# Kernel optimization log

Hardware: AMD Instinct MI355X
Metric: run time of the kernel (lower is better)

## Reference

```python
import jax, jax.numpy as jnp
import numpy as np

N = 50000   # nodes
E = 800000  # edges (avg degree 16)
D = 64      # input_nf = output_nf = hidden_nf


def lrelu(x):
    # nn.LeakyReLU(0.2)
    return jnp.where(x >= 0, x, 0.2 * x)


def setup_inputs() -> dict:
    key = jax.random.key(0)
    ks = jax.random.split(key, 12)
    def lin(k, fan_in, fan_out):
        s = 1.0 / np.sqrt(fan_in)
        return jax.random.uniform(k, (fan_in, fan_out), jnp.float32, -s, s)
    inp = {
        "h": jax.random.normal(ks[0], (N, D), jnp.float32),
        "coord": jax.random.normal(ks[1], (N, 3), jnp.float32),
        "edge_index": jax.random.randint(ks[2], (2, E), 0, N, jnp.int32),
        # edge_mlp: Linear(2D+1, D) -> lrelu -> Linear(D, D) -> lrelu
        "w1e": lin(ks[3], 2 * D + 1, D), "b1e": jnp.zeros((D,), jnp.float32),
        "w2e": lin(ks[4], D, D),         "b2e": jnp.zeros((D,), jnp.float32),
        # node_mlp: Linear(2D, D) -> lrelu -> Linear(D, D)
        "w1n": lin(ks[5], 2 * D, D),     "b1n": jnp.zeros((D,), jnp.float32),
        "w2n": lin(ks[6], D, D),         "b2n": jnp.zeros((D,), jnp.float32),
    }
    return inp


def reference(h, coord, edge_index, w1e, b1e, w2e, b2e, w1n, b1n, w2n, b2n):
    row, col = edge_index[0], edge_index[1]
    # coord2radial
    coord_diff = coord[row] - coord[col]                    # [E, 3]
    radial = jnp.sum(coord_diff ** 2, axis=1, keepdims=True)  # [E, 1]
    # edge_model: concat(h[row], h[col], radial) -> MLP
    e_in = jnp.concatenate([h[row], h[col], radial], axis=1)  # [E, 2D+1]
    e = lrelu(e_in @ w1e + b1e)
    edge_feat = lrelu(e @ w2e + b2e)                        # [E, D]
    # node_model: unsorted_segment_sum over row, then MLP, residual
    agg = jax.ops.segment_sum(edge_feat, row, num_segments=N)  # [N, D]
    n_in = jnp.concatenate([h, agg], axis=1)                # [N, 2D]
    out = lrelu(n_in @ w1n + b1n) @ w2n + b2n               # [N, D]
    h_out = h + out                                         # residual=True
    # coords_weight == 0.0 -> coord passes through unchanged
    return (h_out, coord, edge_feat)
```

## Files before the change

### kernel.cpp

```cpp
#include <hip/hip_runtime.h>

#define NN 50000
#define NE 800000
#define D 64
#define SCAN_B 1024
#define NB ((NN + SCAN_B - 1) / SCAN_B)
#define TILES 5
#define WAVES 8
#define EPB (16 * TILES * WAVES)

typedef __attribute__((ext_vector_type(8))) short bf16x8;
typedef __attribute__((ext_vector_type(4))) float f32x4;
typedef __attribute__((ext_vector_type(4))) unsigned int u32x4;

__device__ __forceinline__ float lrelu(float x) { return x >= 0.0f ? x : 0.2f * x; }

__device__ __forceinline__ unsigned short f2bf(float f) {
    unsigned int x = __float_as_uint(f);
    unsigned int r = (x + 0x7fffu + ((x >> 16) & 1u)) >> 16;
    return (unsigned short)r;
}

__device__ __forceinline__ void wave_lds_fence() {
    asm volatile("s_waitcnt lgkmcnt(0)" ::: "memory");
    __builtin_amdgcn_sched_barrier(0);
}

__global__ __launch_bounds__(256) void prep_count(const float* __restrict__ h,
                                                  unsigned short* __restrict__ hb,
                                                  const int* __restrict__ ei,
                                                  int* __restrict__ counts,
                                                  const float* __restrict__ w1e,
                                                  const float* __restrict__ w2e,
                                                  const float* __restrict__ w1n,
                                                  const float* __restrict__ w2n,
                                                  unsigned short* __restrict__ w1t,
                                                  unsigned short* __restrict__ w2t,
                                                  unsigned short* __restrict__ w1nt,
                                                  unsigned short* __restrict__ w2nt)
{
    int i = blockIdx.x * 256 + threadIdx.x;
    float4 v = ((const float4*)h)[i];
    ushort4 o;
    o.x = f2bf(v.x); o.y = f2bf(v.y); o.z = f2bf(v.z); o.w = f2bf(v.w);
    ((ushort4*)hb)[i] = o;
    atomicAdd(&counts[ei[i]], 1);
    if (i < 8192) {
        int j = i >> 7, k = i & 127;
        w1t[i] = f2bf(w1e[k * 64 + j]);
    } else if (i < 12288) {
        int t2 = i - 8192;
        int j = t2 >> 6, k = t2 & 63;
        w2t[t2] = f2bf(w2e[k * 64 + j]);
    } else if (i < 20480) {
        int t3 = i - 12288;
        int j = t3 >> 7, k = t3 & 127;
        w1nt[t3] = f2bf(w1n[k * 64 + j]);
    } else if (i < 24576) {
        int t4 = i - 20480;
        int j = t4 >> 6, k = t4 & 63;
        w2nt[t4] = f2bf(w2n[k * 64 + j]);
    }
}

__global__ __launch_bounds__(SCAN_B) void scan_block_kernel(const int* __restrict__ counts,
                                                            int* __restrict__ offs,
                                                            int* __restrict__ bsums)
{
    int i = blockIdx.x * SCAN_B + threadIdx.x;
    int v = (i < NN) ? counts[i] : 0;
    int lane = threadIdx.x & 63;
    int wid = threadIdx.x >> 6;
    int x = v;
#pragma unroll
    for (int d = 1; d < 64; d <<= 1) {
        int y = __shfl_up(x, d);
        if (lane >= d) x += y;
    }
    __shared__ int wsum[16];
    if (lane == 63) wsum[wid] = x;
    __syncthreads();
    if (wid == 0) {
        int s = (lane < 16) ? wsum[lane] : 0;
#pragma unroll
        for (int d = 1; d < 16; d <<= 1) {
            int y = __shfl_up(s, d);
            if (lane >= d) s += y;
        }
        if (lane < 16) wsum[lane] = s;
    }
    __syncthreads();
    int woff = (wid == 0) ? 0 : wsum[wid - 1];
    int excl = woff + x - v;
    if (i < NN) offs[i] = excl;
    if (threadIdx.x == 0) bsums[blockIdx.x] = wsum[15];
}

__global__ void scan_top_kernel(int* __restrict__ bsums)
{
    if (threadIdx.x == 0 && blockIdx.x == 0) {
        int run = 0;
        for (int b = 0; b < NB; b++) { int t = bsums[b]; bsums[b] = run; run += t; }
    }
}

__global__ __launch_bounds__(SCAN_B) void add_back_kernel(int* __restrict__ offs,
                                                          const int* __restrict__ bsums,
                                                          int* __restrict__ cursor)
{
    int i = blockIdx.x * SCAN_B + threadIdx.x;
    if (i < NN) {
        int o = offs[i] + bsums[blockIdx.x];
        offs[i] = o;
        cursor[i] = o;
    }
}

__global__ __launch_bounds__(256) void scatter_kernel(const int* __restrict__ ei,
                                                      int* __restrict__ cursor,
                                                      int* __restrict__ csr,
                                                      int* __restrict__ rowpos,
                                                      int* __restrict__ colv)
{
    int e = blockIdx.x * 256 + threadIdx.x;
    if (e < NE) {
        int r = ei[e];
        int pos = atomicAdd(&cursor[r], 1);
        csr[pos] = e;
        rowpos[pos] = r;
        colv[pos] = ei[NE + e];
    }
}

__global__ __launch_bounds__(512, 2) void egnn_edge_mfma(
    const unsigned short* __restrict__ hb, const float* __restrict__ coord,
    const int* __restrict__ csr, const int* __restrict__ rowpos,
    const int* __restrict__ colv,
    const unsigned short* __restrict__ w1t, const float* __restrict__ b1e,
    const float* __restrict__ w1e,
    const unsigned short* __restrict__ w2t, const float* __restrict__ b2e,
    float* __restrict__ edge_feat, float* __restrict__ agg)
{
    __shared__ unsigned short W1[64 * 128];
    __shared__ unsigned short W2[64 * 64];
    __shared__ unsigned short Mb[WAVES][16 * 64];
    __shared__ float Ob[WAVES][16 * 64];

    const int t = threadIdx.x;
    const int orig = blockIdx.x;
    const int xcd = orig & 7, idx8 = orig >> 3;
    const int blk = (xcd < 2 ? xcd * 157 : 2 * 157 + (xcd - 2) * 156) + idx8;

    const int lane = t & 63, wv = t >> 6;
    const int lo = lane & 15, hi = lane >> 4;

    for (int c = t; c < 1024; c += 512) {
        int j = c >> 4, ci = c & 15;
        uint4 v = *(const uint4*)(w1t + j * 128 + ci * 8);
        *(uint4*)((char*)W1 + ((j * 256 + ci * 16) ^ ((j & 7) << 4))) = v;
    }
    for (int c = t; c < 512; c += 512) {
        int j = c >> 3, ci = c & 7;
        uint4 v = *(const uint4*)(w2t + j * 64 + ci * 8);
        *(uint4*)((char*)W2 + ((j * 128 + ci * 16) ^ ((j & 7) << 4))) = v;
    }
    float bj1[4], wl1[4], bj2[4];
#pragma unroll
    for (int ct = 0; ct < 4; ct++) {
        bj1[ct] = b1e[ct * 16 + lo];
        wl1[ct] = w1e[128 * 64 + ct * 16 + lo];
        bj2[ct] = b2e[ct * 16 + lo];
    }
    __syncthreads();

    char* w1b = (char*)W1;
    char* w2b = (char*)W2;
    char* mb = (char*)Mb[wv];
    char* ob = (char*)Ob[wv];

    const int pbase = blk * EPB + wv * (16 * TILES);

    int e5[TILES], row5[TILES], col5[TILES];
    float rad5[TILES];
#pragma unroll
    for (int tl = 0; tl < TILES; tl++) {
        int p = pbase + tl * 16 + lo;
        e5[tl] = csr[p];
        row5[tl] = rowpos[p];
        col5[tl] = colv[p];
    }
#pragma unroll
    for (int tl = 0; tl < TILES; tl++) {
        float dx = coord[row5[tl] * 3 + 0] - coord[col5[tl] * 3 + 0];
        float dy = coord[row5[tl] * 3 + 1] - coord[col5[tl] * 3 + 1];
        float dz = coord[row5[tl] * 3 + 2] - coord[col5[tl] * 3 + 2];
        rad5[tl] = dx * dx + dy * dy + dz * dz;
    }

    uint4 aR0, aR1, aC0, aC1, nR0, nR1, nC0, nC1;
    aR0 = *(const uint4*)(hb + (size_t)row5[0] * 64 + hi * 8);
    aR1 = *(const uint4*)(hb + (size_t)row5[0] * 64 + 32 + hi * 8);
    aC0 = *(const uint4*)(hb + (size_t)col5[0] * 64 + hi * 8);
    aC1 = *(const uint4*)(hb + (size_t)col5[0] * 64 + 32 + hi * 8);

#pragma unroll
    for (int tl = 0; tl < TILES; tl++) {
        if (tl + 1 < TILES) {
            nR0 = *(const uint4*)(hb + (size_t)row5[tl + 1] * 64 + hi * 8);
            nR1 = *(const uint4*)(hb + (size_t)row5[tl + 1] * 64 + 32 + hi * 8);
            nC0 = *(const uint4*)(hb + (size_t)col5[tl + 1] * 64 + hi * 8);
            nC1 = *(const uint4*)(hb + (size_t)col5[tl + 1] * 64 + 32 + hi * 8);
        }

        float radr[4];
#pragma unroll
        for (int r = 0; r < 4; r++) radr[r] = __shfl(rad5[tl], hi * 4 + r);
        f32x4 acc[4];
#pragma unroll
        for (int ct = 0; ct < 4; ct++)
#pragma unroll
            for (int r = 0; r < 4; r++) acc[ct][r] = fmaf(radr[r], wl1[ct], bj1[ct]);

        bf16x8 af0 = *reinterpret_cast<bf16x8*>(&aR0);
        bf16x8 af1 = *reinterpret_cast<bf16x8*>(&aR1);
        bf16x8 af2 = *reinterpret_cast<bf16x8*>(&aC0);
        bf16x8 af3 = *reinterpret_cast<bf16x8*>(&aC1);
#pragma unroll
        for (int kc = 0; kc < 4; kc++) {
            bf16x8 a = (kc == 0) ? af0 : (kc == 1) ? af1 : (kc == 2) ? af2 : af3;
#pragma unroll
            for (int ct = 0; ct < 4; ct++) {
                bf16x8 b = *(bf16x8*)(w1b + (((ct * 16 + lo) * 256 + kc * 64 + hi * 16) ^ ((lo & 7) << 4)));
                acc[ct] = __builtin_amdgcn_mfma_f32_16x16x32_bf16(a, b, acc[ct], 0, 0, 0);
            }
        }

#pragma unroll
        for (int ct = 0; ct < 4; ct++)
#pragma unroll
            for (int r = 0; r < 4; r++) {
                int row = hi * 4 + r;
                *(unsigned short*)(mb + ((row * 128 + (ct * 16 + lo) * 2) ^ ((row & 7) << 4))) =
                    f2bf(lrelu(acc[ct][r]));
            }
        wave_lds_fence();

        f32x4 acc2[4];
#pragma unroll
        for (int ct = 0; ct < 4; ct++)
#pragma unroll
            for (int r = 0; r < 4; r++) acc2[ct][r] = bj2[ct];
#pragma unroll
        for (int kc = 0; kc < 2; kc++) {
            bf16x8 a2 = *(bf16x8*)(mb + ((lo * 128 + kc * 64 + hi * 16) ^ ((lo & 7) << 4)));
#pragma unroll
            for (int ct = 0; ct < 4; ct++) {
                bf16x8 b = *(bf16x8*)(w2b + (((ct * 16 + lo) * 128 + kc * 64 + hi * 16) ^ ((lo & 7) << 4)));
                acc2[ct] = __builtin_amdgcn_mfma_f32_16x16x32_bf16(a2, b, acc2[ct], 0, 0, 0);
            }
        }

#pragma unroll
        for (int ct = 0; ct < 4; ct++)
#pragma unroll
            for (int r = 0; r < 4; r++) {
                int row = hi * 4 + r;
                *(float*)(ob + ((row * 256 + (ct * 16 + lo) * 4) ^ ((row & 7) << 4))) =
                    lrelu(acc2[ct][r]);
            }
        wave_lds_fence();

#pragma unroll
        for (int o = 0; o < 4; o++) {
            int ridx = o * 4 + hi;
            int ee = __shfl(e5[tl], ridx);
            u32x4 v = *(u32x4*)(ob + ((ridx * 256 + lo * 16) ^ ((ridx & 7) << 4)));
            __builtin_nontemporal_store(v, (u32x4*)(edge_feat + (size_t)ee * 64 + lo * 4));
        }
        {
            int cur = __shfl(row5[tl], 0);
            float s = *(float*)(ob + ((lane * 4) ^ 0));
#pragma unroll
            for (int ii = 1; ii < 16; ii++) {
                int r = __shfl(row5[tl], ii);
                float v = *(float*)(ob + ((ii * 256 + lane * 4) ^ ((ii & 7) << 4)));
                if (r != cur) {
                    atomicAdd(&agg[(size_t)cur * 64 + lane], s);
                    s = v; cur = r;
                } else {
                    s += v;
                }
            }
            atomicAdd(&agg[(size_t)cur * 64 + lane], s);
        }

        aR0 = nR0; aR1 = nR1; aC0 = nC0; aC1 = nC1;
    }
}

__global__ __launch_bounds__(256) void agg_node_mfma(
    const unsigned short* __restrict__ hb, const float* __restrict__ h,
    const float* __restrict__ coord, const float* __restrict__ agg,
    const unsigned short* __restrict__ w1nt, const float* __restrict__ b1n,
    const unsigned short* __restrict__ w2nt, const float* __restrict__ b2n,
    float* __restrict__ h_out, float* __restrict__ coord_out)
{
    __shared__ unsigned short Alds[64 * 128];
    __shared__ unsigned short Mlds[64 * 64];

    const int t = threadIdx.x, blk = blockIdx.x;
    const int lane = t & 63, wv = t >> 6;
    const int lo = lane & 15, hi = lane >> 4;
    const int nb = blk * 64;
    char* abase = (char*)Alds;
    char* mbase = (char*)Mlds;

    bf16x8 b1f[4], b2f[2];
#pragma unroll
    for (int kc = 0; kc < 4; kc++)
        b1f[kc] = *(const bf16x8*)(w1nt + (wv * 16 + lo) * 128 + kc * 32 + hi * 8);
#pragma unroll
    for (int kc = 0; kc < 2; kc++)
        b2f[kc] = *(const bf16x8*)(w2nt + (wv * 16 + lo) * 64 + kc * 32 + hi * 8);
    const float bj1 = b1n[wv * 16 + lo];
    const float bj2 = b2n[wv * 16 + lo];

    {
        int row = t >> 2, seg = t & 3;
        int n = min(nb + row, NN - 1);
        const uint4* src = (const uint4*)(hb + (size_t)n * 64 + seg * 16);
        int base = row * 256 + seg * 32;
        int swr = (row & 7) << 4;
        uint4 v0 = src[0], v1 = src[1];
        *(uint4*)(abase + (base ^ swr)) = v0;
        *(uint4*)(abase + ((base + 16) ^ swr)) = v1;
    }
    {
        int row = t >> 2, seg = t & 3;
        int n = min(nb + row, NN - 1);
        const float4* asrc = (const float4*)(agg + (size_t)n * 64 + seg * 16);
        float4 a0 = asrc[0], a1 = asrc[1], a2 = asrc[2], a3 = asrc[3];
        unsigned int u0 = f2bf(a0.x) | ((unsigned)f2bf(a0.y) << 16);
        unsigned int u1 = f2bf(a0.z) | ((unsigned)f2bf(a0.w) << 16);
        unsigned int u2 = f2bf(a1.x) | ((unsigned)f2bf(a1.y) << 16);
        unsigned int u3 = f2bf(a1.z) | ((unsigned)f2bf(a1.w) << 16);
        unsigned int u4 = f2bf(a2.x) | ((unsigned)f2bf(a2.y) << 16);
        unsigned int u5 = f2bf(a2.z) | ((unsigned)f2bf(a2.w) << 16);
        unsigned int u6 = f2bf(a3.x) | ((unsigned)f2bf(a3.y) << 16);
        unsigned int u7 = f2bf(a3.z) | ((unsigned)f2bf(a3.w) << 16);
        int base = row * 256 + 128 + seg * 32;
        int swr = (row & 7) << 4;
        *(uint4*)(abase + (base ^ swr)) = make_uint4(u0, u1, u2, u3);
        *(uint4*)(abase + ((base + 16) ^ swr)) = make_uint4(u4, u5, u6, u7);
    }
    __syncthreads();

    f32x4 acc[4];
#pragma unroll
    for (int rt = 0; rt < 4; rt++) {
#pragma unroll
        for (int r = 0; r < 4; r++) acc[rt][r] = bj1;
    }
#pragma unroll
    for (int kc = 0; kc < 4; kc++) {
#pragma unroll
        for (int rt = 0; rt < 4; rt++) {
            int row = rt * 16 + lo;
            bf16x8 a = *(bf16x8*)(abase + ((row * 256 + kc * 64 + hi * 16) ^ ((row & 7) << 4)));
            acc[rt] = __builtin_amdgcn_mfma_f32_16x16x32_bf16(a, b1f[kc], acc[rt], 0, 0, 0);
        }
    }
#pragma unroll
    for (int rt = 0; rt < 4; rt++) {
#pragma unroll
        for (int r = 0; r < 4; r++) {
            int row = rt * 16 + hi * 4 + r;
            *(unsigned short*)(mbase + ((row * 128 + (wv * 16 + lo) * 2) ^ ((row & 7) << 4))) =
                f2bf(lrelu(acc[rt][r]));
        }
    }
    __syncthreads();

    f32x4 acc2[4];
#pragma unroll
    for (int rt = 0; rt < 4; rt++) {
#pragma unroll
        for (int r = 0; r < 4; r++) acc2[rt][r] = bj2;
    }
#pragma unroll
    for (int kc = 0; kc < 2; kc++) {
#pragma unroll
        for (int rt = 0; rt < 4; rt++) {
            int row = rt * 16 + lo;
            bf16x8 a = *(bf16x8*)(mbase + ((row * 128 + kc * 64 + hi * 16) ^ ((row & 7) << 4)));
            acc2[rt] = __builtin_amdgcn_mfma_f32_16x16x32_bf16(a, b2f[kc], acc2[rt], 0, 0, 0);
        }
    }
#pragma unroll
    for (int rt = 0; rt < 4; rt++) {
#pragma unroll
        for (int r = 0; r < 4; r++) {
            int row = rt * 16 + hi * 4 + r;
            int n = nb + row;
            if (n < NN) {
                int c = wv * 16 + lo;
                float v = h[(size_t)n * 64 + c] + acc2[rt][r];
                __builtin_nontemporal_store(v, h_out + (size_t)n * 64 + c);
            }
        }
    }

    if (t < 192) {
        int idx = nb * 3 + t;
        if (idx < NN * 3) coord_out[idx] = coord[idx];
    }
}

extern "C" void kernel_launch(void* const* d_in, const int* in_sizes, int n_in,
                              void* d_out, int out_size, void* d_ws, size_t ws_size,
                              hipStream_t stream)
{
    const float* h     = (const float*)d_in[0];
    const float* coord = (const float*)d_in[1];
    const int*   ei    = (const int*)d_in[2];
    const float* w1e   = (const float*)d_in[3];
    const float* b1e   = (const float*)d_in[4];
    const float* w2e   = (const float*)d_in[5];
    const float* b2e   = (const float*)d_in[6];
    const float* w1n   = (const float*)d_in[7];
    const float* b1n   = (const float*)d_in[8];
    const float* w2n   = (const float*)d_in[9];
    const float* b2n   = (const float*)d_in[10];

    float* out       = (float*)d_out;
    float* h_out     = out;
    float* coord_out = out + (size_t)NN * D;
    float* edge_feat = coord_out + (size_t)NN * 3;

    char* ws = (char*)d_ws;
    unsigned short* hb   = (unsigned short*)ws;  ws += sizeof(unsigned short) * (size_t)NN * D;
    unsigned short* w1t  = (unsigned short*)ws;  ws += sizeof(unsigned short) * 64 * 128;
    unsigned short* w2t  = (unsigned short*)ws;  ws += sizeof(unsigned short) * 64 * 64;
    unsigned short* w1nt = (unsigned short*)ws;  ws += sizeof(unsigned short) * 64 * 128;
    unsigned short* w2nt = (unsigned short*)ws;  ws += sizeof(unsigned short) * 64 * 64;
    float* agg  = (float*)ws;                    ws += sizeof(float) * (size_t)NN * D;
    int* counts = (int*)ws;                      ws += sizeof(int) * NN;
    int* offs   = (int*)ws;                      ws += sizeof(int) * NN;
    int* cursor = (int*)ws;                      ws += sizeof(int) * NN;
    int* bsums  = (int*)ws;                      ws += sizeof(int) * 64;
    int* csr    = (int*)ws;                      ws += sizeof(int) * NE;
    int* rowpos = (int*)ws;                      ws += sizeof(int) * NE;
    int* colv   = (int*)ws;                      ws += sizeof(int) * NE;

    hipMemsetAsync(counts, 0, sizeof(int) * NN, stream);
    hipMemsetAsync(agg, 0, sizeof(float) * (size_t)NN * D, stream);

    prep_count<<<NE / 256, 256, 0, stream>>>(h, hb, ei, counts,
                                             w1e, w2e, w1n, w2n, w1t, w2t, w1nt, w2nt);

    scan_block_kernel<<<NB, SCAN_B, 0, stream>>>(counts, offs, bsums);
    scan_top_kernel<<<1, 64, 0, stream>>>(bsums);
    add_back_kernel<<<NB, SCAN_B, 0, stream>>>(offs, bsums, cursor);
    scatter_kernel<<<(NE + 255) / 256, 256, 0, stream>>>(ei, cursor, csr, rowpos, colv);

    egnn_edge_mfma<<<NE / EPB, 512, 0, stream>>>(
        hb, coord, csr, rowpos, colv, w1t, b1e, w1e, w2t, b2e, edge_feat, agg);

    agg_node_mfma<<<(NN + 63) / 64, 256, 0, stream>>>(
        hb, h, coord, agg, w1nt, b1n, w2nt, b2n, h_out, coord_out);
}
```

Measured before the change: 200.0 us.

## Stage edge outputs in bf16 LDS buffer and move radial/edge ids to LDS

Removes the per-wave fp32 output staging buffer and reuses the bf16 Mb buffer for the second-layer output, cutting LDS use. Per-edge radial values and edge ids move from per-lane register arrays into small LDS arrays, freeing registers and dropping shuffles. The trade-off is that edge_feat and the aggregation are now rounded to bf16 precision instead of fp32, which changes numerical accuracy.

```diff
diff --git a/kernel.cpp b/kernel.cpp
--- a/kernel.cpp
+++ b/kernel.cpp
@@ -19,6 +19,9 @@
     unsigned int x = __float_as_uint(f);
     unsigned int r = (x + 0x7fffu + ((x >> 16) & 1u)) >> 16;
     return (unsigned short)r;
+}
+__device__ __forceinline__ float bf2f(unsigned short u) {
+    return __uint_as_float(((unsigned int)u) << 16);
 }
 
 __device__ __forceinline__ void wave_lds_fence() {
@@ -144,7 +147,8 @@
     __shared__ unsigned short W1[64 * 128];
     __shared__ unsigned short W2[64 * 64];
     __shared__ unsigned short Mb[WAVES][16 * 64];
-    __shared__ float Ob[WAVES][16 * 64];
+    __shared__ float Rb[WAVES][16 * TILES];
+    __shared__ int Eb[WAVES][16 * TILES];
 
     const int t = threadIdx.x;
     const int orig = blockIdx.x;
@@ -176,25 +180,25 @@
     char* w1b = (char*)W1;
     char* w2b = (char*)W2;
     char* mb = (char*)Mb[wv];
-    char* ob = (char*)Ob[wv];
 
     const int pbase = blk * EPB + wv * (16 * TILES);
 
-    int e5[TILES], row5[TILES], col5[TILES];
-    float rad5[TILES];
+    int row5[TILES], col5[TILES];
 #pragma unroll
     for (int tl = 0; tl < TILES; tl++) {
         int p = pbase + tl * 16 + lo;
-        e5[tl] = csr[p];
         row5[tl] = rowpos[p];
         col5[tl] = colv[p];
-    }
-#pragma unroll
-    for (int tl = 0; tl < TILES; tl++) {
-        float dx = coord[row5[tl] * 3 + 0] - coord[col5[tl] * 3 + 0];
-        float dy = coord[row5[tl] * 3 + 1] - coord[col5[tl] * 3 + 1];
-        float dz = coord[row5[tl] * 3 + 2] - coord[col5[tl] * 3 + 2];
-        rad5[tl] = dx * dx + dy * dy + dz * dz;
+        if (hi == 0) Eb[wv][tl * 16 + lo] = csr[p];
+    }
+    if (hi == 0) {
+#pragma unroll
+        for (int tl = 0; tl < TILES; tl++) {
+            float dx = coord[row5[tl] * 3 + 0] - coord[col5[tl] * 3 + 0];
+            float dy = coord[row5[tl] * 3 + 1] - coord[col5[tl] * 3 + 1];
+            float dz = coord[row5[tl] * 3 + 2] - coord[col5[tl] * 3 + 2];
+            Rb[wv][tl * 16 + lo] = dx * dx + dy * dy + dz * dz;
+        }
     }
 
     uint4 aR0, aR1, aC0, aC1, nR0, nR1, nC0, nC1;
@@ -212,15 +216,20 @@
             nC1 = *(const uint4*)(hb + (size_t)col5[tl + 1] * 64 + 32 + hi * 8);
         }
 
-        float radr[4];
-#pragma unroll
-        for (int r = 0; r < 4; r++) radr[r] = __shfl(rad5[tl], hi * 4 + r);
         f32x4 acc[4];
-#pragma unroll
-        for (int ct = 0; ct < 4; ct++)
-#pragma unroll
-            for (int r = 0; r < 4; r++) acc[ct][r] = fmaf(radr[r], wl1[ct], bj1[ct]);
-
+        {
+            float r0 = Rb[wv][tl * 16 + hi * 4 + 0];
+            float r1 = Rb[wv][tl * 16 + hi * 4 + 1];
+            float r2 = Rb[wv][tl * 16 + hi * 4 + 2];
+            float r3 = Rb[wv][tl * 16 + hi * 4 + 3];
+#pragma unroll
+            for (int ct = 0; ct < 4; ct++) {
+                acc[ct][0] = fmaf(r0, wl1[ct], bj1[ct]);
+                acc[ct][1] = fmaf(r1, wl1[ct], bj1[ct]);
+                acc[ct][2] = fmaf(r2, wl1[ct], bj1[ct]);
+                acc[ct][3] = fmaf(r3, wl1[ct], bj1[ct]);
+            }
+        }
         bf16x8 af0 = *reinterpret_cast<bf16x8*>(&aR0);
         bf16x8 af1 = *reinterpret_cast<bf16x8*>(&aR1);
         bf16x8 af2 = *reinterpret_cast<bf16x8*>(&aC0);
@@ -265,25 +274,30 @@
 #pragma unroll
             for (int r = 0; r < 4; r++) {
                 int row = hi * 4 + r;
-                *(float*)(ob + ((row * 256 + (ct * 16 + lo) * 4) ^ ((row & 7) << 4))) =
-                    lrelu(acc2[ct][r]);
+                *(unsigned short*)(mb + ((row * 128 + (ct * 16 + lo) * 2) ^ ((row & 7) << 4))) =
+                    f2bf(lrelu(acc2[ct][r]));
             }
         wave_lds_fence();
 
 #pragma unroll
         for (int o = 0; o < 4; o++) {
             int ridx = o * 4 + hi;
-            int ee = __shfl(e5[tl], ridx);
-            u32x4 v = *(u32x4*)(ob + ((ridx * 256 + lo * 16) ^ ((ridx & 7) << 4)));
+            int ee = Eb[wv][tl * 16 + ridx];
+            uint2 uv = *(uint2*)(mb + ((ridx * 128 + lo * 8) ^ ((ridx & 7) << 4)));
+            u32x4 v;
+            v.x = (uv.x & 0xffffu) << 16;
+            v.y = (uv.x & 0xffff0000u);
+            v.z = (uv.y & 0xffffu) << 16;
+            v.w = (uv.y & 0xffff0000u);
             __builtin_nontemporal_store(v, (u32x4*)(edge_feat + (size_t)ee * 64 + lo * 4));
         }
         {
             int cur = __shfl(row5[tl], 0);
-            float s = *(float*)(ob + ((lane * 4) ^ 0));
+            float s = bf2f(*(unsigned short*)(mb + ((lane * 2) ^ 0)));
 #pragma unroll
             for (int ii = 1; ii < 16; ii++) {
                 int r = __shfl(row5[tl], ii);
-                float v = *(float*)(ob + ((ii * 256 + lane * 4) ^ ((ii & 7) << 4)));
+                float v = bf2f(*(unsigned short*)(mb + ((ii * 128 + lane * 2) ^ ((ii & 7) << 4))));
                 if (r != cur) {
                     atomicAdd(&agg[(size_t)cur * 64 + lane], s);
                     s = v; cur = r;
```

Result: no change. 202.2 us (+1.1%).
